# Optimization experiments

Measured on AMD Instinct MI355X. Metric: run time of the kernel, lower is better.

## Reference

```python
import jax, jax.numpy as jnp
import numpy as np

# Mamba2 config (from init_kwargs + mamba_ssm Mamba2 defaults)
D_MODEL = 256
D_STATE = 16
D_CONV = 4
EXPAND = 2
HEADDIM = 64                      # Mamba2 default
D_INNER = EXPAND * D_MODEL        # 512
NHEADS = D_INNER // HEADDIM       # 8
CONV_DIM = D_INNER + 2 * D_STATE  # 544 (ngroups=1)
D_IN_PROJ = 2 * D_INNER + 2 * D_STATE + NHEADS  # 1064
B, H, W = 8, 64, 64
EPS = 1e-5


def setup_inputs() -> dict:
    key = jax.random.key(0)
    ks = jax.random.split(key, 8)
    x = jax.random.normal(ks[0], (B, D_MODEL, H, W), jnp.float32)
    ln_w = jnp.ones((D_MODEL,), jnp.float32)
    ln_b = jnp.zeros((D_MODEL,), jnp.float32)
    in_proj_w = jax.random.normal(ks[1], (D_IN_PROJ, D_MODEL), jnp.float32) * (D_MODEL ** -0.5)
    conv_w = jax.random.normal(ks[2], (CONV_DIM, D_CONV), jnp.float32) * (D_CONV ** -0.5)
    conv_b = jnp.zeros((CONV_DIM,), jnp.float32)
    dt = jax.random.uniform(ks[3], (NHEADS,), jnp.float32, 1e-3, 0.1)
    dt_bias = dt + jnp.log(-jnp.expm1(-dt))  # inverse softplus
    A_log = jnp.log(jax.random.uniform(ks[4], (NHEADS,), jnp.float32, 1.0, 16.0))
    D = jnp.ones((NHEADS,), jnp.float32)
    rms_w = jnp.ones((D_INNER,), jnp.float32)
    out_proj_w = jax.random.normal(ks[5], (D_MODEL, D_INNER), jnp.float32) * (D_INNER ** -0.5)
    return dict(x=x, ln_w=ln_w, ln_b=ln_b, in_proj_w=in_proj_w, conv_w=conv_w,
                conv_b=conv_b, dt_bias=dt_bias, A_log=A_log, D=D, rms_w=rms_w,
                out_proj_w=out_proj_w)


def reference(x, ln_w, ln_b, in_proj_w, conv_w, conv_b, dt_bias, A_log, D, rms_w, out_proj_w):
    Bb, C, Hh, Ww = x.shape
    L = Hh * Ww
    # (B,C,H,W) -> (B,L,C)
    xs = x.transpose(0, 2, 3, 1).reshape(Bb, L, C)
    # pre-LayerNorm
    mu = jnp.mean(xs, -1, keepdims=True)
    var = jnp.mean((xs - mu) ** 2, -1, keepdims=True)
    xn = (xs - mu) * jax.lax.rsqrt(var + EPS) * ln_w + ln_b
    # input projection -> z | xBC | dt
    zxbcdt = xn @ in_proj_w.T
    z = zxbcdt[..., :D_INNER]
    xBC = zxbcdt[..., D_INNER:D_INNER + CONV_DIM]
    dt = jax.nn.softplus(zxbcdt[..., D_INNER + CONV_DIM:] + dt_bias)  # (B,L,NH)
    # causal depthwise conv1d (kernel D_CONV) + SiLU
    xp = jnp.pad(xBC, ((0, 0), (D_CONV - 1, 0), (0, 0)))
    conv = conv_b
    for k in range(D_CONV):  # small fixed kernel loop
        conv = conv + xp[:, k:k + L, :] * conv_w[:, k]
    xBC = jax.nn.silu(conv)
    xh = xBC[..., :D_INNER].reshape(Bb, L, NHEADS, HEADDIM)
    Bm = xBC[..., D_INNER:D_INNER + D_STATE]   # (B,L,N)
    Cm = xBC[..., D_INNER + D_STATE:]          # (B,L,N)
    A = -jnp.exp(A_log)                        # (NH,)
    dA = jnp.exp(dt * A)                       # (B,L,NH)
    dtx = dt[..., None] * xh                   # (B,L,NH,P)

    def step(h, inp):
        dA_t, dtx_t, B_t, C_t = inp
        # h: (B,NH,P,N)
        h = dA_t[:, :, None, None] * h + dtx_t[..., None] * B_t[:, None, None, :]
        y = jnp.einsum('bhpn,bn->bhp', h, C_t)
        return h, y

    h0 = jnp.zeros((Bb, NHEADS, HEADDIM, D_STATE), xs.dtype)
    _, ys = jax.lax.scan(step, h0, (dA.transpose(1, 0, 2), dtx.transpose(1, 0, 2, 3),
                                    Bm.transpose(1, 0, 2), Cm.transpose(1, 0, 2)))
    y = ys.transpose(1, 0, 2, 3) + D[:, None] * xh   # (B,L,NH,P)
    y = y.reshape(Bb, L, D_INNER)
    # gated RMSNorm (norm_before_gate=False): rmsnorm(y * silu(z)) * w
    y = y * jax.nn.silu(z)
    y = y * jax.lax.rsqrt(jnp.mean(y * y, -1, keepdims=True) + EPS) * rms_w
    out = y @ out_proj_w.T
    out = out.reshape(Bb, Hh, Ww, C).transpose(0, 3, 1, 2) + x
    return out
```

## Files before the change

### kernel.cpp

```cpp
#include <hip/hip_runtime.h>
#include <cstdint>

typedef unsigned short u16;
typedef unsigned int u32;
typedef u16 u16x8 __attribute__((ext_vector_type(8)));
typedef short short8 __attribute__((ext_vector_type(8)));
typedef float f32x4 __attribute__((ext_vector_type(4)));

__device__ __forceinline__ float bf2f(u16 u){ return __uint_as_float(((u32)u)<<16); }
__device__ __forceinline__ u16 f2bf(float f){
  u32 x = __float_as_uint(f);
  return (u16)((x + 0x7fffu + ((x>>16)&1u)) >> 16);
}
__device__ __forceinline__ float siluf(float v){ return v/(1.f + __expf(-v)); }


__global__ __launch_bounds__(256) void k0_wprep(const float* __restrict__ w1,
                                                const float* __restrict__ w2,
                                                u16* __restrict__ w1b, u16* __restrict__ w2b){
  u32 idx = blockIdx.x*256u + threadIdx.x;
  const u32 W1N = 1152u*256u;
  const u32 W2N = 256u*512u;
  if (idx < W1N){
    u32 n = idx >> 8;
    w1b[idx] = (n < 1064u) ? f2bf(w1[idx]) : (u16)0;
  } else if (idx < W1N + W2N){
    u32 j = idx - W1N;
    w2b[j] = f2bf(w2[j]);
  }
}

__global__ __launch_bounds__(256) void k1_ln(const float* __restrict__ x,
                                             const float* __restrict__ ln_w, const float* __restrict__ ln_b,
                                             const float* __restrict__ w1,
                                             u16* __restrict__ xnb, float* __restrict__ dtr){
  __shared__ float tile[256][33];
  __shared__ float mu_s[32], rs_s[32];
  const int b  = blockIdx.y;
  const int l0 = blockIdx.x*32;
  const int tid = threadIdx.x;
  const size_t xbase = (size_t)b*256*4096;
  const int cl = tid>>5;
  const int ll = tid&31;
  for (int cc=0; cc<256; cc+=8){
    int c = cc + cl;
    tile[c][ll] = x[xbase + (size_t)c*4096 + l0 + ll];
  }
  __syncthreads();
  const int lane = tid&63, wave = tid>>6;
  const int lidx = wave*8 + (lane&7);
  const int c0 = (lane>>3)*32;
  float s=0.f, ss=0.f;
  for (int c=c0; c<c0+32; ++c){ float v = tile[c][lidx]; s += v; ss += v*v; }
  for (int off=8; off<64; off<<=1){ s += __shfl_xor(s, off); ss += __shfl_xor(ss, off); }
  float mu = s*(1.f/256.f);
  float var = ss*(1.f/256.f) - mu*mu;
  float rs = rsqrtf(var + 1e-5f);
  if ((lane>>3)==0){ mu_s[lidx]=mu; rs_s[lidx]=rs; }
  __syncthreads();
  {
    const int c = tid;
    const float lw = ln_w[c], lb = ln_b[c];
    for (int l=0; l<32; ++l){
      float v = (tile[c][l]-mu_s[l])*rs_s[l]*lw + lb;
      xnb[((size_t)b*4096 + l0 + l)*256 + c] = f2bf(v);
    }
  }
  {
    const int r = tid>>3, j = tid&7;
    const float* wr = w1 + (size_t)(1056+j)*256;
    const float mur = mu_s[r], rsr = rs_s[r];
    float acc = 0.f;
    for (int c=0; c<256; ++c){
      float v = (tile[c][r]-mur)*rsr*ln_w[c] + ln_b[c];
      acc += v*wr[c];
    }
    dtr[((size_t)b*4096 + l0 + r)*8 + j] = acc;
  }
}

__global__ __launch_bounds__(256) void k2_gemm1(const u16* __restrict__ A, const u16* __restrict__ W,
                                                u16* __restrict__ zb, float* __restrict__ xbc){
  __shared__ u16 sA[128*40];
  __shared__ u16 sW[128*40];
  const int tid = threadIdx.x, lane = tid&63, wave = tid>>6;
  const size_t m0 = (size_t)blockIdx.y*128;
  const int n0 = blockIdx.x*128;
  const int wm = (wave>>1)*64, wn = (wave&1)*64;
  f32x4 acc[4][4] = {};
  const int fr = lane&15, kc = (lane>>4)*8;
  for (int k0=0; k0<256; k0+=32){
    #pragma unroll
    for (int j=0; j<2; ++j){
      int ch = j*256 + tid, r = ch>>2, co = (ch&3)*8;
      *(u16x8*)&sA[r*40+co] = *(const u16x8*)&A[(m0+r)*256 + k0 + co];
      *(u16x8*)&sW[r*40+co] = *(const u16x8*)&W[(size_t)(n0+r)*256 + k0 + co];
    }
    __syncthreads();
    short8 af[4], bf4[4];
    #pragma unroll
    for (int fm=0; fm<4; ++fm) af[fm]  = *(short8*)&sA[(wm+fm*16+fr)*40 + kc];
    #pragma unroll
    for (int fn=0; fn<4; ++fn) bf4[fn] = *(short8*)&sW[(wn+fn*16+fr)*40 + kc];
    #pragma unroll
    for (int fm=0; fm<4; ++fm)
      #pragma unroll
      for (int fn=0; fn<4; ++fn)
        acc[fm][fn] = __builtin_amdgcn_mfma_f32_16x16x32_bf16(af[fm],bf4[fn],acc[fm][fn],0,0,0);
    __syncthreads();
  }
  #pragma unroll
  for (int fm=0; fm<4; ++fm)
    #pragma unroll
    for (int fn=0; fn<4; ++fn){
      int rb = wm + fm*16 + ((lane>>4)<<2);
      int col = n0 + wn + fn*16 + (lane&15);
      #pragma unroll
      for (int i=0; i<4; ++i){
        size_t m = m0 + rb + i;
        float v = acc[fm][fn][i];
        if (col < 512)        zb[m*512 + col] = f2bf(v);
        else if (col < 1056)  xbc[m*544 + (col-512)] = v;
      }
    }
}

__global__ __launch_bounds__(512) void k4_phase1(const float* __restrict__ xbc, const float* __restrict__ dtr,
                                                 const float* __restrict__ conv_w, const float* __restrict__ conv_b,
                                                 const float* __restrict__ dt_bias, const float* __restrict__ A_log,
                                                 float* __restrict__ hend, float* __restrict__ aprod){
  __shared__ float raw[67][16];
  __shared__ float sB[64][16];
  __shared__ float sdt[64][8];
  const int b = blockIdx.y, ck = blockIdx.x;
  const int tid = threadIdx.x, h = tid>>6, lane = tid&63;
  const int m0 = b*4096 + ck*64;
  for (int i=tid; i<67*16; i+=512){
    int r=i>>4, n=i&15; int l = ck*64 - 3 + r;
    raw[r][n] = (l>=0) ? xbc[(size_t)(b*4096+l)*544 + 512 + n] : 0.f;
  }
  { int t=tid>>3, hh=tid&7;
    float dr = dtr[(size_t)(m0+t)*8 + hh] + dt_bias[hh];
    sdt[t][hh] = (dr > 20.f) ? dr : log1pf(__expf(dr));
  }
  __syncthreads();
  for (int i=tid; i<64*16; i+=512){
    int t=i>>4, n=i&15; int c = 512+n;
    float a = conv_b[c] + conv_w[c*4+0]*raw[t][n] + conv_w[c*4+1]*raw[t+1][n]
            + conv_w[c*4+2]*raw[t+2][n] + conv_w[c*4+3]*raw[t+3][n];
    sB[t][n] = siluf(a);
  }
  __syncthreads();
  const int c = h*64 + lane;
  const float w0=conv_w[c*4], w1=conv_w[c*4+1], w2=conv_w[c*4+2], w3=conv_w[c*4+3];
  const float cb = conv_b[c];
  const int lb = ck*64;
  float xm3 = (lb-3>=0) ? xbc[(size_t)(m0-3)*544 + c] : 0.f;
  float xm2 = (lb-2>=0) ? xbc[(size_t)(m0-2)*544 + c] : 0.f;
  float xm1 = (lb-1>=0) ? xbc[(size_t)(m0-1)*544 + c] : 0.f;
  const float Ah = -__expf(A_log[h]);
  float hreg[16];
  #pragma unroll
  for (int n=0;n<16;++n) hreg[n]=0.f;
  float cum = 1.f;
  #pragma unroll 4
  for (int t=0; t<64; ++t){
    float xc = xbc[(size_t)(m0+t)*544 + c];
    float cv = cb + w0*xm3 + w1*xm2 + w2*xm1 + w3*xc;
    float xv = siluf(cv);
    xm3=xm2; xm2=xm1; xm1=xc;
    float dtva = sdt[t][h];
    float a = __expf(dtva*Ah);
    float dtx = dtva*xv;
    #pragma unroll
    for (int n=0;n<16;++n) hreg[n] = a*hreg[n] + dtx*sB[t][n];
    cum *= a;
  }
  size_t base = (((size_t)(b*8+h)*64 + ck)*64 + lane)*16;
  #pragma unroll
  for (int n=0;n<16;++n) hend[base+n] = hreg[n];
  if (lane==0) aprod[(b*8+h)*64 + ck] = cum;
}

__global__ __launch_bounds__(64) void k5_phase2(const float* __restrict__ hend, const float* __restrict__ aprod,
                                                float* __restrict__ hs){
  const int bh = blockIdx.x;
  const int lane = threadIdx.x;
  float hr[16];
  #pragma unroll
  for (int n=0;n<16;++n) hr[n]=0.f;
  for (int ck=0; ck<64; ++ck){
    size_t base = (((size_t)bh*64 + ck)*64 + lane)*16;
    float a = aprod[bh*64 + ck];
    #pragma unroll
    for (int n=0;n<16;++n) hs[base+n] = hr[n];
    #pragma unroll
    for (int n=0;n<16;++n) hr[n] = a*hr[n] + hend[base+n];
  }
}

__global__ __launch_bounds__(512) void k6_phase3(const float* __restrict__ xbc, const float* __restrict__ dtr,
                                                 const float* __restrict__ conv_w, const float* __restrict__ conv_b,
                                                 const float* __restrict__ dt_bias, const float* __restrict__ A_log,
                                                 const float* __restrict__ Dp,
                                                 const float* __restrict__ hs, u16* __restrict__ ybh){
  __shared__ float raw[67][32];
  __shared__ float sB[64][16];
  __shared__ float sC[64][16];
  __shared__ float sdt[64][8];
  const int b = blockIdx.y, ck = blockIdx.x;
  const int tid = threadIdx.x, h = tid>>6, lane = tid&63;
  const int m0 = b*4096 + ck*64;
  for (int i=tid; i<67*32; i+=512){
    int r=i>>5, n=i&31; int l = ck*64 - 3 + r;
    raw[r][n] = (l>=0) ? xbc[(size_t)(b*4096+l)*544 + 512 + n] : 0.f;
  }
  { int t=tid>>3, hh=tid&7;
    float dr = dtr[(size_t)(m0+t)*8 + hh] + dt_bias[hh];
    sdt[t][hh] = (dr > 20.f) ? dr : log1pf(__expf(dr));
  }
  __syncthreads();
  for (int i=tid; i<64*32; i+=512){
    int t=i>>5, n=i&31; int c = 512+n;
    float a = conv_b[c] + conv_w[c*4+0]*raw[t][n] + conv_w[c*4+1]*raw[t+1][n]
            + conv_w[c*4+2]*raw[t+2][n] + conv_w[c*4+3]*raw[t+3][n];
    float s = siluf(a);
    if (n < 16) sB[t][n] = s; else sC[t][n-16] = s;
  }
  __syncthreads();
  const int c = h*64 + lane;
  const float w0=conv_w[c*4], w1=conv_w[c*4+1], w2=conv_w[c*4+2], w3=conv_w[c*4+3];
  const float cb = conv_b[c];
  const int lb = ck*64;
  float xm3 = (lb-3>=0) ? xbc[(size_t)(m0-3)*544 + c] : 0.f;
  float xm2 = (lb-2>=0) ? xbc[(size_t)(m0-2)*544 + c] : 0.f;
  float xm1 = (lb-1>=0) ? xbc[(size_t)(m0-1)*544 + c] : 0.f;
  const float Ah = -__expf(A_log[h]);
  const float Dh = Dp[h];
  float hreg[16];
  size_t hbase = (((size_t)(b*8+h)*64 + ck)*64 + lane)*16;
  #pragma unroll
  for (int n=0;n<16;++n) hreg[n] = hs[hbase+n];
  #pragma unroll 4
  for (int t=0; t<64; ++t){
    float xc = xbc[(size_t)(m0+t)*544 + c];
    float cv = cb + w0*xm3 + w1*xm2 + w2*xm1 + w3*xc;
    float xv = siluf(cv);
    xm3=xm2; xm2=xm1; xm1=xc;
    float dtva = sdt[t][h];
    float a = __expf(dtva*Ah);
    float dtx = dtva*xv;
    float yv = 0.f;
    #pragma unroll
    for (int n=0;n<16;++n){ hreg[n] = a*hreg[n] + dtx*sB[t][n]; yv += hreg[n]*sC[t][n]; }
    ybh[(size_t)(m0+t)*512 + c] = f2bf(yv + Dh*xv);
  }
}

__global__ __launch_bounds__(256) void k7_rms(const u16* __restrict__ y, const u16* __restrict__ zb,
                                              const float* __restrict__ rms_w, u16* __restrict__ ynb){
  const int m = blockIdx.x*4 + (threadIdx.x>>6);
  const int lane = threadIdx.x&63;
  const size_t base = (size_t)m*512 + lane*8;
  u16x8 yv = *(const u16x8*)&y[base];
  u16x8 zv = *(const u16x8*)&zb[base];
  float g[8];
  float ssum = 0.f;
  #pragma unroll
  for (int j=0;j<8;++j){
    float zf = bf2f(zv[j]);
    float sig = 1.f/(1.f + __expf(-zf));
    g[j] = bf2f(yv[j]) * (zf*sig);
    ssum += g[j]*g[j];
  }
  for (int off=1; off<64; off<<=1) ssum += __shfl_xor(ssum, off);
  float rs = rsqrtf(ssum*(1.f/512.f) + 1e-5f);
  u16x8 o;
  #pragma unroll
  for (int j=0;j<8;++j) o[j] = f2bf(g[j]*rs*rms_w[lane*8+j]);
  *(u16x8*)&ynb[base] = o;
}

__global__ __launch_bounds__(256) void k8_gemm2(const u16* __restrict__ A, const u16* __restrict__ W,
                                                const float* __restrict__ xres, float* __restrict__ out){
  __shared__ float smem[4*64*65];
  u16* sA = (u16*)smem;
  u16* sW = ((u16*)smem) + 128*40;
  const int tid = threadIdx.x, lane = tid&63, wave = tid>>6;
  const size_t m0 = (size_t)blockIdx.y*128;
  const int n0 = blockIdx.x*128;
  const int wm = (wave>>1)*64, wn = (wave&1)*64;
  f32x4 acc[4][4] = {};
  const int fr = lane&15, kc = (lane>>4)*8;
  for (int k0=0; k0<512; k0+=32){
    #pragma unroll
    for (int j=0; j<2; ++j){
      int ch = j*256 + tid, r = ch>>2, co = (ch&3)*8;
      *(u16x8*)&sA[r*40+co] = *(const u16x8*)&A[(m0+r)*512 + k0 + co];
      *(u16x8*)&sW[r*40+co] = *(const u16x8*)&W[(size_t)(n0+r)*512 + k0 + co];
    }
    __syncthreads();
    short8 af[4], bf4[4];
    #pragma unroll
    for (int fm=0; fm<4; ++fm) af[fm]  = *(short8*)&sA[(wm+fm*16+fr)*40 + kc];
    #pragma unroll
    for (int fn=0; fn<4; ++fn) bf4[fn] = *(short8*)&sW[(wn+fn*16+fr)*40 + kc];
    #pragma unroll
    for (int fm=0; fm<4; ++fm)
      #pragma unroll
      for (int fn=0; fn<4; ++fn)
        acc[fm][fn] = __builtin_amdgcn_mfma_f32_16x16x32_bf16(af[fm],bf4[fn],acc[fm][fn],0,0,0);
    __syncthreads();
  }
  float* T = smem + wave*(64*65);
  #pragma unroll
  for (int fm=0; fm<4; ++fm)
    #pragma unroll
    for (int fn=0; fn<4; ++fn){
      int rr = fm*16 + ((lane>>4)<<2);
      int cc = fn*16 + (lane&15);
      #pragma unroll
      for (int i=0; i<4; ++i) T[(rr+i)*65 + cc] = acc[fm][fn][i];
    }
  __syncthreads();
  const int bb = (int)(m0>>12);
  const int lbase = (int)(m0&4095) + wm;
  for (int cc=0; cc<64; ++cc){
    int col = n0 + wn + cc;
    size_t o = ((size_t)bb*256 + col)*4096 + lbase + lane;
    out[o] = T[lane*65 + cc] + xres[o];
  }
}

extern "C" void kernel_launch(void* const* d_in, const int* in_sizes, int n_in,
                              void* d_out, int out_size, void* d_ws, size_t ws_size,
                              hipStream_t stream){
  const float* x        = (const float*)d_in[0];
  const float* ln_w     = (const float*)d_in[1];
  const float* ln_b     = (const float*)d_in[2];
  const float* in_proj  = (const float*)d_in[3];
  const float* conv_w   = (const float*)d_in[4];
  const float* conv_b   = (const float*)d_in[5];
  const float* dt_bias  = (const float*)d_in[6];
  const float* A_log    = (const float*)d_in[7];
  const float* Dp       = (const float*)d_in[8];
  const float* rms_w    = (const float*)d_in[9];
  const float* out_proj = (const float*)d_in[10];
  float* out = (float*)d_out;

  char* ws = (char*)d_ws;
  const size_t o_w1   = 0;
  const size_t o_w2   = 589824;
  const size_t o_xn   = 851968;
  const size_t o_z    = 17629184;
  const size_t o_xbc  = 51183616;
  const size_t o_dtr  = 122486784;
  const size_t o_hend = 123535360;
  const size_t o_hs   = 140312576;
  const size_t o_ap   = 157089792;
  const size_t o_ybh  = 157106176;
  const size_t NEED   = 190660608;
  if (ws_size < NEED) return;

  u16*   w1b  = (u16*)(ws + o_w1);
  u16*   w2b  = (u16*)(ws + o_w2);
  u16*   xnb  = (u16*)(ws + o_xn);
  u16*   zbuf = (u16*)(ws + o_z);
  float* xbc  = (float*)(ws + o_xbc);
  float* dtr  = (float*)(ws + o_dtr);
  float* hend = (float*)(ws + o_hend);
  float* hsb  = (float*)(ws + o_hs);
  float* ap   = (float*)(ws + o_ap);
  u16*   ybh  = (u16*)(ws + o_ybh);
  u16*   ynb  = (u16*)(ws + o_hend);

  k0_wprep<<<1664, 256, 0, stream>>>(in_proj, out_proj, w1b, w2b);
  k1_ln<<<dim3(128, 8), 256, 0, stream>>>(x, ln_w, ln_b, in_proj, xnb, dtr);
  k2_gemm1<<<dim3(9, 256), 256, 0, stream>>>(xnb, w1b, zbuf, xbc);
  k4_phase1<<<dim3(64, 8), 512, 0, stream>>>(xbc, dtr, conv_w, conv_b, dt_bias, A_log, hend, ap);
  k5_phase2<<<64, 64, 0, stream>>>(hend, ap, hsb);
  k6_phase3<<<dim3(64, 8), 512, 0, stream>>>(xbc, dtr, conv_w, conv_b, dt_bias, A_log, Dp, hsb, ybh);
  k7_rms<<<8192, 256, 0, stream>>>(ybh, zbuf, rms_w, ynb);
  k8_gemm2<<<dim3(2, 256), 256, 0, stream>>>(ynb, w2b, x, out);
}
```

Baseline: 317.2 us.

## Reformulate chunked SSM scan as SSD matrix products on MFMA with bf16 xBC

Replaces the per-timestep sequential recurrence in both chunk kernels with the SSD chunked formulation. Within each chunk the end states and outputs come from bf16 MFMA matmuls (C·Bᵀ Gram matrix with a causal decay mask, X·B for states, C·h0 for the inter-chunk term), and a wave-shuffle prefix sum of dt·A supplies the decay factors. The xBC intermediate is now stored as bf16 instead of fp32, which halves that traffic, and blocks are split per half of the heads for more parallelism. The cost is lower precision in the states, the Gram matrix and the mask factors, which risks accuracy drift, along with heavier LDS use per block.

```diff
diff --git a/kernel.cpp b/kernel.cpp
--- a/kernel.cpp
+++ b/kernel.cpp
@@ -4,6 +4,7 @@
 typedef unsigned short u16;
 typedef unsigned int u32;
 typedef u16 u16x8 __attribute__((ext_vector_type(8)));
+typedef u16 u16x4 __attribute__((ext_vector_type(4)));
 typedef short short8 __attribute__((ext_vector_type(8)));
 typedef float f32x4 __attribute__((ext_vector_type(4)));
 
@@ -80,7 +81,7 @@
 }
 
 __global__ __launch_bounds__(256) void k2_gemm1(const u16* __restrict__ A, const u16* __restrict__ W,
-                                                u16* __restrict__ zb, float* __restrict__ xbc){
+                                                u16* __restrict__ zb, u16* __restrict__ xbcb){
   __shared__ u16 sA[128*40];
   __shared__ u16 sW[128*40];
   const int tid = threadIdx.x, lane = tid&63, wave = tid>>6;
@@ -120,66 +121,87 @@
         size_t m = m0 + rb + i;
         float v = acc[fm][fn][i];
         if (col < 512)        zb[m*512 + col] = f2bf(v);
-        else if (col < 1056)  xbc[m*544 + (col-512)] = v;
+        else if (col < 1056)  xbcb[m*544 + (col-512)] = f2bf(v);
       }
     }
 }
 
-__global__ __launch_bounds__(512) void k4_phase1(const float* __restrict__ xbc, const float* __restrict__ dtr,
-                                                 const float* __restrict__ conv_w, const float* __restrict__ conv_b,
-                                                 const float* __restrict__ dt_bias, const float* __restrict__ A_log,
-                                                 float* __restrict__ hend, float* __restrict__ aprod){
-  __shared__ float raw[67][16];
-  __shared__ float sB[64][16];
-  __shared__ float sdt[64][8];
-  const int b = blockIdx.y, ck = blockIdx.x;
-  const int tid = threadIdx.x, h = tid>>6, lane = tid&63;
+__global__ __launch_bounds__(256) void kU(const u16* __restrict__ xbcb, const float* __restrict__ dtr,
+                                          const float* __restrict__ conv_w, const float* __restrict__ conv_b,
+                                          const float* __restrict__ dt_bias, const float* __restrict__ A_log,
+                                          float* __restrict__ hend, float* __restrict__ aprod){
+  __shared__ char lds[44816];
+  float* rawB = (float*)(lds + 0);
+  u16*   BcT  = (u16*)(lds + 4560);
+  float* wl   = (float*)(lds + 6864);
+  const int ck = blockIdx.x, b = blockIdx.y, half = blockIdx.z;
+  const int tid = threadIdx.x, lane = tid&63, hh = tid>>6;
+  const int h = half*4 + hh;
   const int m0 = b*4096 + ck*64;
-  for (int i=tid; i<67*16; i+=512){
-    int r=i>>4, n=i&15; int l = ck*64 - 3 + r;
-    raw[r][n] = (l>=0) ? xbc[(size_t)(b*4096+l)*544 + 512 + n] : 0.f;
-  }
-  { int t=tid>>3, hh=tid&7;
-    float dr = dtr[(size_t)(m0+t)*8 + hh] + dt_bias[hh];
-    sdt[t][hh] = (dr > 20.f) ? dr : log1pf(__expf(dr));
-  }
-  __syncthreads();
-  for (int i=tid; i<64*16; i+=512){
-    int t=i>>4, n=i&15; int c = 512+n;
-    float a = conv_b[c] + conv_w[c*4+0]*raw[t][n] + conv_w[c*4+1]*raw[t+1][n]
-            + conv_w[c*4+2]*raw[t+2][n] + conv_w[c*4+3]*raw[t+3][n];
-    sB[t][n] = siluf(a);
-  }
-  __syncthreads();
-  const int c = h*64 + lane;
-  const float w0=conv_w[c*4], w1=conv_w[c*4+1], w2=conv_w[c*4+2], w3=conv_w[c*4+3];
-  const float cb = conv_b[c];
-  const int lb = ck*64;
-  float xm3 = (lb-3>=0) ? xbc[(size_t)(m0-3)*544 + c] : 0.f;
-  float xm2 = (lb-2>=0) ? xbc[(size_t)(m0-2)*544 + c] : 0.f;
-  float xm1 = (lb-1>=0) ? xbc[(size_t)(m0-1)*544 + c] : 0.f;
-  const float Ah = -__expf(A_log[h]);
-  float hreg[16];
-  #pragma unroll
-  for (int n=0;n<16;++n) hreg[n]=0.f;
-  float cum = 1.f;
-  #pragma unroll 4
-  for (int t=0; t<64; ++t){
-    float xc = xbc[(size_t)(m0+t)*544 + c];
-    float cv = cb + w0*xm3 + w1*xm2 + w2*xm1 + w3*xc;
-    float xv = siluf(cv);
-    xm3=xm2; xm2=xm1; xm1=xc;
-    float dtva = sdt[t][h];
-    float a = __expf(dtva*Ah);
-    float dtx = dtva*xv;
-    #pragma unroll
-    for (int n=0;n<16;++n) hreg[n] = a*hreg[n] + dtx*sB[t][n];
-    cum *= a;
-  }
-  size_t base = (((size_t)(b*8+h)*64 + ck)*64 + lane)*16;
-  #pragma unroll
-  for (int n=0;n<16;++n) hend[base+n] = hreg[n];
-  if (lane==0) aprod[(b*8+h)*64 + ck] = cum;
+  u16* XW = (u16*)(lds + 7888 + hh*9232);
+  for (int i=tid; i<67*16; i+=256){
+    int r = i>>4, n = i&15; int l = ck*64 - 3 + r;
+    rawB[r*17+n] = (l>=0) ? bf2f(xbcb[(size_t)(b*4096+l)*544 + 512 + n]) : 0.f;
+  }
+  {
+    int t = lane;
+    float dr = dtr[(size_t)(m0+t)*8 + h] + dt_bias[h];
+    float dt = (dr > 20.f) ? dr : log1pf(__expf(dr));
+    float Ah = -__expf(A_log[h]);
+    float v = dt*Ah;
+    #pragma unroll
+    for (int off=1; off<64; off<<=1){ float p = __shfl_up(v, off); if (lane >= off) v += p; }
+    float scT = __shfl(v, 63);
+    wl[hh*64 + t] = dt * __expf(scT - v);
+    if (lane==0) aprod[(b*8+h)*64 + ck] = __expf(scT);
+  }
+  __syncthreads();
+  for (int i=tid; i<16*64; i+=256){
+    int n = i>>6, s = i&63;
+    int c = 512+n;
+    float a = conv_b[c] + conv_w[c*4+0]*rawB[s*17+n] + conv_w[c*4+1]*rawB[(s+1)*17+n]
+            + conv_w[c*4+2]*rawB[(s+2)*17+n] + conv_w[c*4+3]*rawB[(s+3)*17+n];
+    BcT[n*72 + s] = f2bf(siluf(a));
+  }
+  {
+    const int c = h*64 + lane;
+    const float w0=conv_w[c*4], w1=conv_w[c*4+1], w2=conv_w[c*4+2], w3=conv_w[c*4+3];
+    const float cb = conv_b[c];
+    const int lb = ck*64;
+    float xm3 = (lb>=3)? bf2f(xbcb[(size_t)(m0-3)*544 + c]) : 0.f;
+    float xm2 = (lb>=2)? bf2f(xbcb[(size_t)(m0-2)*544 + c]) : 0.f;
+    float xm1 = (lb>=1)? bf2f(xbcb[(size_t)(m0-1)*544 + c]) : 0.f;
+    #pragma unroll 4
+    for (int t=0; t<64; t+=2){
+      float xc0 = bf2f(xbcb[(size_t)(m0+t)*544 + c]);
+      float s0v = siluf(cb + w0*xm3 + w1*xm2 + w2*xm1 + w3*xc0) * wl[hh*64 + t];
+      xm3=xm2; xm2=xm1; xm1=xc0;
+      float xc1 = bf2f(xbcb[(size_t)(m0+t+1)*544 + c]);
+      float s1v = siluf(cb + w0*xm3 + w1*xm2 + w2*xm1 + w3*xc1) * wl[hh*64 + t+1];
+      xm3=xm2; xm2=xm1; xm1=xc1;
+      *(u32*)&XW[lane*72 + t] = (u32)f2bf(s0v) | ((u32)f2bf(s1v)<<16);
+    }
+  }
+  __syncthreads();
+  const int fr = lane&15, g = lane>>4;
+  f32x4 acc[4] = {};
+  #pragma unroll
+  for (int ks=0; ks<2; ++ks){
+    short8 bfr = *(short8*)&BcT[fr*72 + ks*32 + g*8];
+    #pragma unroll
+    for (int ti=0; ti<4; ++ti){
+      short8 afr = *(short8*)&XW[(ti*16+fr)*72 + ks*32 + g*8];
+      acc[ti] = __builtin_amdgcn_mfma_f32_16x16x32_bf16(afr, bfr, acc[ti], 0,0,0);
+    }
+  }
+  size_t hb = ((size_t)((b*8+h)*64 + ck))*64;
+  #pragma unroll
+  for (int ti=0; ti<4; ++ti)
+    #pragma unroll
+    for (int i=0; i<4; ++i){
+      int p = ti*16 + g*4 + i;
+      hend[(hb + p)*16 + fr] = acc[ti][i];
+    }
 }
 
 __global__ __launch_bounds__(64) void k5_phase2(const float* __restrict__ hend, const float* __restrict__ aprod,
@@ -199,61 +221,177 @@
   }
 }
 
-__global__ __launch_bounds__(512) void k6_phase3(const float* __restrict__ xbc, const float* __restrict__ dtr,
-                                                 const float* __restrict__ conv_w, const float* __restrict__ conv_b,
-                                                 const float* __restrict__ dt_bias, const float* __restrict__ A_log,
-                                                 const float* __restrict__ Dp,
-                                                 const float* __restrict__ hs, u16* __restrict__ ybh){
-  __shared__ float raw[67][32];
-  __shared__ float sB[64][16];
-  __shared__ float sC[64][16];
-  __shared__ float sdt[64][8];
-  const int b = blockIdx.y, ck = blockIdx.x;
-  const int tid = threadIdx.x, h = tid>>6, lane = tid&63;
+__global__ __launch_bounds__(256) void kY(const u16* __restrict__ xbcb, const float* __restrict__ dtr,
+                                          const float* __restrict__ conv_w, const float* __restrict__ conv_b,
+                                          const float* __restrict__ dt_bias, const float* __restrict__ A_log,
+                                          const float* __restrict__ Dp, const float* __restrict__ hs,
+                                          u16* __restrict__ ybh){
+  __shared__ char lds[58560];
+  u16*   G     = (u16*)(lds + 0);
+  float* rawBC = (float*)(lds + 0);
+  u16*   Cc    = (u16*)(lds + 9216);
+  u16*   Bc    = (u16*)(lds + 14336);
+  float* scs   = (float*)(lds + 19456);
+  float* dth   = (float*)(lds + 20544);
+  const int ck = blockIdx.x, b = blockIdx.y, half = blockIdx.z;
+  const int tid = threadIdx.x, lane = tid&63, hh = tid>>6;
+  const int h = half*4 + hh;
   const int m0 = b*4096 + ck*64;
-  for (int i=tid; i<67*32; i+=512){
-    int r=i>>5, n=i&31; int l = ck*64 - 3 + r;
-    raw[r][n] = (l>=0) ? xbc[(size_t)(b*4096+l)*544 + 512 + n] : 0.f;
-  }
-  { int t=tid>>3, hh=tid&7;
-    float dr = dtr[(size_t)(m0+t)*8 + hh] + dt_bias[hh];
-    sdt[t][hh] = (dr > 20.f) ? dr : log1pf(__expf(dr));
-  }
-  __syncthreads();
-  for (int i=tid; i<64*32; i+=512){
-    int t=i>>5, n=i&31; int c = 512+n;
-    float a = conv_b[c] + conv_w[c*4+0]*raw[t][n] + conv_w[c*4+1]*raw[t+1][n]
-            + conv_w[c*4+2]*raw[t+2][n] + conv_w[c*4+3]*raw[t+3][n];
-    float s = siluf(a);
-    if (n < 16) sB[t][n] = s; else sC[t][n-16] = s;
-  }
-  __syncthreads();
-  const int c = h*64 + lane;
-  const float w0=conv_w[c*4], w1=conv_w[c*4+1], w2=conv_w[c*4+2], w3=conv_w[c*4+3];
-  const float cb = conv_b[c];
-  const int lb = ck*64;
-  float xm3 = (lb-3>=0) ? xbc[(size_t)(m0-3)*544 + c] : 0.f;
-  float xm2 = (lb-2>=0) ? xbc[(size_t)(m0-2)*544 + c] : 0.f;
-  float xm1 = (lb-1>=0) ? xbc[(size_t)(m0-1)*544 + c] : 0.f;
-  const float Ah = -__expf(A_log[h]);
-  const float Dh = Dp[h];
-  float hreg[16];
-  size_t hbase = (((size_t)(b*8+h)*64 + ck)*64 + lane)*16;
-  #pragma unroll
-  for (int n=0;n<16;++n) hreg[n] = hs[hbase+n];
-  #pragma unroll 4
-  for (int t=0; t<64; ++t){
-    float xc = xbc[(size_t)(m0+t)*544 + c];
-    float cv = cb + w0*xm3 + w1*xm2 + w2*xm1 + w3*xc;
-    float xv = siluf(cv);
-    xm3=xm2; xm2=xm1; xm1=xc;
-    float dtva = sdt[t][h];
-    float a = __expf(dtva*Ah);
-    float dtx = dtva*xv;
-    float yv = 0.f;
-    #pragma unroll
-    for (int n=0;n<16;++n){ hreg[n] = a*hreg[n] + dtx*sB[t][n]; yv += hreg[n]*sC[t][n]; }
-    ybh[(size_t)(m0+t)*512 + c] = f2bf(yv + Dh*xv);
+  u16* XT = (u16*)(lds + 21632 + hh*9232);
+  for (int i=tid; i<67*32; i+=256){
+    int r = i>>5, n = i&31; int l = ck*64 - 3 + r;
+    rawBC[r*33+n] = (l>=0) ? bf2f(xbcb[(size_t)(b*4096+l)*544 + 512 + n]) : 0.f;
+  }
+  {
+    int t = lane;
+    float dr = dtr[(size_t)(m0+t)*8 + h] + dt_bias[h];
+    float dt = (dr > 20.f) ? dr : log1pf(__expf(dr));
+    float Ah = -__expf(A_log[h]);
+    float v = dt*Ah;
+    #pragma unroll
+    for (int off=1; off<64; off<<=1){ float p = __shfl_up(v, off); if (lane >= off) v += p; }
+    dth[hh*68 + t] = dt;
+    scs[hh*68 + t] = v;
+  }
+  {
+    const int c = h*64 + lane;
+    const float w0=conv_w[c*4], w1=conv_w[c*4+1], w2=conv_w[c*4+2], w3=conv_w[c*4+3];
+    const float cb = conv_b[c];
+    const int lb = ck*64;
+    float xm3 = (lb>=3)? bf2f(xbcb[(size_t)(m0-3)*544 + c]) : 0.f;
+    float xm2 = (lb>=2)? bf2f(xbcb[(size_t)(m0-2)*544 + c]) : 0.f;
+    float xm1 = (lb>=1)? bf2f(xbcb[(size_t)(m0-1)*544 + c]) : 0.f;
+    #pragma unroll 4
+    for (int t=0; t<64; t+=2){
+      float xc0 = bf2f(xbcb[(size_t)(m0+t)*544 + c]);
+      float s0v = siluf(cb + w0*xm3 + w1*xm2 + w2*xm1 + w3*xc0);
+      xm3=xm2; xm2=xm1; xm1=xc0;
+      float xc1 = bf2f(xbcb[(size_t)(m0+t+1)*544 + c]);
+      float s1v = siluf(cb + w0*xm3 + w1*xm2 + w2*xm1 + w3*xc1);
+      xm3=xm2; xm2=xm1; xm1=xc1;
+      *(u32*)&XT[lane*72 + t] = (u32)f2bf(s0v) | ((u32)f2bf(s1v)<<16);
+    }
+  }
+  __syncthreads();
+  for (int i=tid; i<64*32; i+=256){
+    int s = i>>5, n = i&31;
+    int c = 512 + n;
+    float a = conv_b[c] + conv_w[c*4+0]*rawBC[s*33+n] + conv_w[c*4+1]*rawBC[(s+1)*33+n]
+            + conv_w[c*4+2]*rawBC[(s+2)*33+n] + conv_w[c*4+3]*rawBC[(s+3)*33+n];
+    u16 v = f2bf(siluf(a));
+    if (n < 16) Bc[s*40 + n] = v; else Cc[s*40 + (n-16)] = v;
+  }
+  for (int i=tid; i<64*16; i+=256){
+    int s = i>>4, n = i&15;
+    Bc[s*40 + 16 + n] = 0; Cc[s*40 + 16 + n] = 0;
+  }
+  __syncthreads();
+  const int fr = lane&15, g = lane>>4;
+  #define GFRAG(TI,SJ) { \
+    short8 ca = *(short8*)&Cc[((TI)*16+fr)*40 + g*8]; \
+    short8 bb = *(short8*)&Bc[((SJ)*16+fr)*40 + g*8]; \
+    f32x4 d = {}; \
+    d = __builtin_amdgcn_mfma_f32_16x16x32_bf16(ca, bb, d, 0,0,0); \
+    G[((TI)*16 + g*4 + 0)*72 + (SJ)*16 + fr] = f2bf(d[0]); \
+    G[((TI)*16 + g*4 + 1)*72 + (SJ)*16 + fr] = f2bf(d[1]); \
+    G[((TI)*16 + g*4 + 2)*72 + (SJ)*16 + fr] = f2bf(d[2]); \
+    G[((TI)*16 + g*4 + 3)*72 + (SJ)*16 + fr] = f2bf(d[3]); }
+  if      (hh==0){ GFRAG(0,0) GFRAG(2,1) GFRAG(3,2) }
+  else if (hh==1){ GFRAG(1,0) GFRAG(2,2) GFRAG(3,3) }
+  else if (hh==2){ GFRAG(1,1) GFRAG(3,0) }
+  else           { GFRAG(2,0) GFRAG(3,1) }
+  #undef GFRAG
+  __syncthreads();
+  f32x4 acc[4][4] = {};
+  {
+    size_t hsbase = ((size_t)((b*8+h)*64 + ck))*64*16;
+    short8 h0f[4];
+    #pragma unroll
+    for (int pj=0; pj<4; ++pj){
+      short8 hf = {0,0,0,0,0,0,0,0};
+      if (g < 2){
+        int p = pj*16 + fr;
+        f32x4 lo = *(const f32x4*)&hs[hsbase + p*16 + g*8];
+        f32x4 hi = *(const f32x4*)&hs[hsbase + p*16 + g*8 + 4];
+        #pragma unroll
+        for (int kk=0; kk<4; ++kk){ hf[kk] = (short)f2bf(lo[kk]); hf[kk+4] = (short)f2bf(hi[kk]); }
+      }
+      h0f[pj] = hf;
+    }
+    #pragma unroll
+    for (int ti=0; ti<4; ++ti){
+      short8 ca = *(short8*)&Cc[(ti*16+fr)*40 + g*8];
+      #pragma unroll
+      for (int pj=0; pj<4; ++pj)
+        acc[ti][pj] = __builtin_amdgcn_mfma_f32_16x16x32_bf16(ca, h0f[pj], acc[ti][pj], 0,0,0);
+    }
+  }
+  #pragma unroll
+  for (int ti=0; ti<4; ++ti)
+    #pragma unroll
+    for (int i=0; i<4; ++i){
+      float pt = __expf(scs[hh*68 + ti*16 + g*4 + i]);
+      #pragma unroll
+      for (int pj=0; pj<4; ++pj) acc[ti][pj][i] *= pt;
+    }
+  #pragma unroll
+  for (int ks=0; ks<2; ++ks){
+    short8 xf[4];
+    #pragma unroll
+    for (int pj=0; pj<4; ++pj) xf[pj] = *(short8*)&XT[(pj*16+fr)*72 + ks*32 + g*8];
+    #pragma unroll
+    for (int ti=0; ti<4; ++ti){
+      if (ks*32 > ti*16+15) continue;
+      int t = ti*16 + fr;
+      float sct = scs[hh*68 + t];
+      f32x4 sc0 = *(f32x4*)&scs[hh*68 + ks*32 + g*8];
+      f32x4 sc1 = *(f32x4*)&scs[hh*68 + ks*32 + g*8 + 4];
+      f32x4 dt0 = *(f32x4*)&dth[hh*68 + ks*32 + g*8];
+      f32x4 dt1 = *(f32x4*)&dth[hh*68 + ks*32 + g*8 + 4];
+      u16x8 g8 = *(u16x8*)&G[t*72 + ks*32 + g*8];
+      short8 mf;
+      #pragma unroll
+      for (int kk=0; kk<8; ++kk){
+        int s = ks*32 + g*8 + kk;
+        float sv = (kk<4) ? sc0[kk] : sc1[kk-4];
+        float dv = (kk<4) ? dt0[kk] : dt1[kk-4];
+        float m = (s <= t) ? bf2f(g8[kk]) * __expf(sct - sv) * dv : 0.f;
+        mf[kk] = (short)f2bf(m);
+      }
+      #pragma unroll
+      for (int pj=0; pj<4; ++pj)
+        acc[ti][pj] = __builtin_amdgcn_mfma_f32_16x16x32_bf16(mf, xf[pj], acc[ti][pj], 0,0,0);
+    }
+  }
+  {
+    const float Dh = Dp[h];
+    #pragma unroll
+    for (int ti=0; ti<4; ++ti)
+      #pragma unroll
+      for (int pj=0; pj<4; ++pj){
+        int p = pj*16 + fr;
+        u16x4 xv = *(u16x4*)&XT[p*72 + ti*16 + g*4];
+        #pragma unroll
+        for (int i=0; i<4; ++i) acc[ti][pj][i] += Dh * bf2f(xv[i]);
+      }
+  }
+  #pragma unroll
+  for (int ti=0; ti<4; ++ti)
+    #pragma unroll
+    for (int pj=0; pj<4; ++pj)
+      #pragma unroll
+      for (int i=0; i<4; ++i)
+        XT[(ti*16 + g*4 + i)*72 + pj*16 + fr] = f2bf(acc[ti][pj][i]);
+  __syncthreads();
+  {
+    const int hl = lane>>4;
+    const u16* R = (const u16*)(lds + 21632 + hl*9232);
+    #pragma unroll
+    for (int tt=0; tt<16; ++tt){
+      int t = hh*16 + tt;
+      u16x4 v = *(const u16x4*)&R[t*72 + (lane&15)*4];
+      *(u16x4*)&ybh[(size_t)(m0+t)*512 + half*256 + lane*4] = v;
+    }
   }
 }
 
@@ -353,20 +491,20 @@
   const size_t o_w2   = 589824;
   const size_t o_xn   = 851968;
   const size_t o_z    = 17629184;
-  const size_t o_xbc  = 51183616;
-  const size_t o_dtr  = 122486784;
-  const size_t o_hend = 123535360;
-  const size_t o_hs   = 140312576;
-  const size_t o_ap   = 157089792;
-  const size_t o_ybh  = 157106176;
-  const size_t NEED   = 190660608;
+  const size_t o_xbcb = 51183616;
+  const size_t o_dtr  = 86835200;
+  const size_t o_hend = 87883776;
+  const size_t o_hs   = 104660992;
+  const size_t o_ap   = 121438208;
+  const size_t o_ybh  = 121454592;
+  const size_t NEED   = 155009024;
   if (ws_size < NEED) return;
 
   u16*   w1b  = (u16*)(ws + o_w1);
   u16*   w2b  = (u16*)(ws + o_w2);
   u16*   xnb  = (u16*)(ws + o_xn);
   u16*   zbuf = (u16*)(ws + o_z);
-  float* xbc  = (float*)(ws + o_xbc);
+  u16*   xbcb = (u16*)(ws + o_xbcb);
   float* dtr  = (float*)(ws + o_dtr);
   float* hend = (float*)(ws + o_hend);
   float* hsb  = (float*)(ws + o_hs);
@@ -376,10 +514,10 @@
 
   k0_wprep<<<1664, 256, 0, stream>>>(in_proj, out_proj, w1b, w2b);
   k1_ln<<<dim3(128, 8), 256, 0, stream>>>(x, ln_w, ln_b, in_proj, xnb, dtr);
-  k2_gemm1<<<dim3(9, 256), 256, 0, stream>>>(xnb, w1b, zbuf, xbc);
-  k4_phase1<<<dim3(64, 8), 512, 0, stream>>>(xbc, dtr, conv_w, conv_b, dt_bias, A_log, hend, ap);
+  k2_gemm1<<<dim3(9, 256), 256, 0, stream>>>(xnb, w1b, zbuf, xbcb);
+  kU<<<dim3(64, 8, 2), 256, 0, stream>>>(xbcb, dtr, conv_w, conv_b, dt_bias, A_log, hend, ap);
   k5_phase2<<<64, 64, 0, stream>>>(hend, ap, hsb);
-  k6_phase3<<<dim3(64, 8), 512, 0, stream>>>(xbc, dtr, conv_w, conv_b, dt_bias, A_log, Dp, hsb, ybh);
+  kY<<<dim3(64, 8, 2), 256, 0, stream>>>(xbcb, dtr, conv_w, conv_b, dt_bias, A_log, Dp, hsb, ybh);
   k7_rms<<<8192, 256, 0, stream>>>(ybh, zbuf, rms_w, ynb);
   k8_gemm2<<<dim3(2, 256), 256, 0, stream>>>(ynb, w2b, x, out);
 }
```

New measurement: 293.4 us. 1.08x faster.
